# Kernel tuning notes

Measured on AMD Instinct MI355X. Metric: run time of the kernel, lower is better.

## Reference

```python
import jax, jax.numpy as jnp
import numpy as np
from jax import lax

B, S, D = 2, 1024, 1024
N = 16            # mamba state dim
EXPAND = 2
DI = EXPAND * D   # inner dim 2048
K = 4             # depthwise conv kernel
H = 16            # soliton heads
DH = D // H
DT_RANK = D // 16
SOL_DT = 0.1      # soliton integration step


def _ln(x, g, b):
    mu = jnp.mean(x, -1, keepdims=True)
    var = jnp.var(x, -1, keepdims=True)
    return (x - mu) / jnp.sqrt(var + 1e-5) * g + b


def setup_inputs() -> dict:
    key = jax.random.key(0)
    ks = jax.random.split(key, 12)
    def nrm(k, sh, sc=0.02):
        return jax.random.normal(k, sh, jnp.float32) * sc
    return {
        'x': nrm(ks[0], (B, S, D), 1.0),
        'ln1_g': jnp.ones(D), 'ln1_b': jnp.zeros(D),
        'W_in': nrm(ks[1], (D, 2 * DI)), 'b_in': jnp.zeros(2 * DI),
        'conv_w': nrm(ks[2], (DI, K), 0.1), 'conv_b': jnp.zeros(DI),
        'W_xp': nrm(ks[3], (DI, DT_RANK + 2 * N)),
        'W_dt': nrm(ks[4], (DT_RANK, DI), 0.1),
        'b_dt': jnp.full((DI,), -4.6),  # softplus(-4.6) ~ 0.01 init dt
        'A_log': jnp.log(jnp.broadcast_to(jnp.arange(1, N + 1, dtype=jnp.float32), (DI, N))),
        'D_skip': jnp.ones(DI),
        'W_out': nrm(ks[5], (DI, D)), 'b_out': jnp.zeros(D),
        'ln2_g': jnp.ones(D), 'ln2_b': jnp.zeros(D),
        'W_si': nrm(ks[6], (D, D)), 'b_si': jnp.zeros(D),
        'gates': nrm(ks[7], (H, 3), 0.1),   # per-head weights for [sine-Gordon, KdV, Heimburg-Jackson]
        'alpha': nrm(ks[8], (H,), 0.1),     # HJ nonlinearity coefficient
        'W_so': nrm(ks[9], (D, D)), 'b_so': jnp.zeros(D),
    }


def _forward(x, ln1_g, ln1_b, W_in, b_in, conv_w, conv_b, W_xp, W_dt, b_dt,
             A_log, D_skip, W_out, b_out, ln2_g, ln2_b, W_si, b_si,
             gates, alpha, W_so, b_so):
    b, s, d = x.shape
    # ---- Mamba mixer branch ----
    u = _ln(x, ln1_g, ln1_b)
    xz = u @ W_in + b_in                                   # [b,s,2*DI]
    xp, z = jnp.split(xz, 2, axis=-1)                      # [b,s,DI] each
    # causal depthwise conv along sequence
    xt = xp.transpose(0, 2, 1)                             # [b,DI,s]
    yc = lax.conv_general_dilated(xt, conv_w[:, None, :], (1,), [(K - 1, 0)],
                                  feature_group_count=DI,
                                  dimension_numbers=('NCW', 'OIW', 'NCW'))
    xc = jax.nn.silu(yc.transpose(0, 2, 1) + conv_b)       # [b,s,DI]
    dbc = xc @ W_xp
    dtr, Bs, Cs = jnp.split(dbc, [DT_RANK, DT_RANK + N], axis=-1)
    dt = jax.nn.softplus(dtr @ W_dt + b_dt)                # [b,s,DI]
    A = -jnp.exp(A_log)                                    # [DI,N]
    dA = jnp.exp(dt[..., None] * A)                        # [b,s,DI,N]
    dBx = (dt * xc)[..., None] * Bs[:, :, None, :]         # [b,s,DI,N]

    def step(h, inp):
        dA_t, dBx_t, C_t = inp
        h = dA_t * h + dBx_t                               # [b,DI,N]
        y = jnp.einsum('bdn,bn->bd', h, C_t)
        return h, y

    h0 = jnp.zeros((b, DI, N), x.dtype)
    xs = (dA.transpose(1, 0, 2, 3), dBx.transpose(1, 0, 2, 3), Cs.transpose(1, 0, 2))
    _, ys = lax.scan(step, h0, xs)
    y = ys.transpose(1, 0, 2)                              # [b,s,DI]
    y = (y + xc * D_skip) * jax.nn.silu(z)
    x = x + y @ W_out + b_out

    # ---- Soliton interaction branch ----
    v = _ln(x, ln2_g, ln2_b)
    uu = (v @ W_si + b_si).reshape(b, s, H, DH)
    up = jnp.pad(uu, ((0, 0), (2, 2), (0, 0), (0, 0)), mode='edge')
    ux = (up[:, 3:-1] - up[:, 1:-3]) * 0.5                 # central 1st derivative
    uxx = up[:, 3:-1] - 2.0 * uu + up[:, 1:-3]
    uxxx = (up[:, 4:] - 2.0 * up[:, 3:-1] + 2.0 * up[:, 1:-3] - up[:, :-4]) * 0.5
    sg = jnp.sin(uu)                                       # sine-Gordon
    kdv = -6.0 * uu * ux - uxxx                            # KdV
    hj = (1.0 + alpha[None, None, :, None] * uu) * uxx     # Heimburg-Jackson
    du = (gates[None, None, :, 0:1] * sg
          + gates[None, None, :, 1:2] * kdv
          + gates[None, None, :, 2:3] * hj)
    sol = (SOL_DT * du).reshape(b, s, d) @ W_so + b_so
    return x + sol


def reference(x, ln1_g, ln1_b, W_in, b_in, conv_w, conv_b, W_xp, W_dt, b_dt,
              A_log, D_skip, W_out, b_out, ln2_g, ln2_b, W_si, b_si,
              gates, alpha, W_so, b_so):
    return _forward(x, ln1_g, ln1_b, W_in, b_in, conv_w, conv_b, W_xp, W_dt, b_dt,
                    A_log, D_skip, W_out, b_out, ln2_g, ln2_b, W_si, b_si,
                    gates, alpha, W_so, b_so)
```

## Files before the change

### kernel.cpp

```cpp
#include <hip/hip_runtime.h>
#include <hip/hip_bf16.h>
#include <math.h>

typedef unsigned short u16;
typedef unsigned int u32;
typedef __attribute__((ext_vector_type(8))) short short8;
typedef __attribute__((ext_vector_type(4))) float f32x4;

constexpr int CB = 2;
constexpr int CS = 1024;
constexpr int CD = 1024;
constexpr int CDI = 2048;
constexpr int CNC2 = 64;
constexpr int CL2 = 16;

__device__ inline u16 f2bf(float v) {
  __hip_bfloat16 h = __float2bfloat16(v);
  return *reinterpret_cast<u16*>(&h);
}
__device__ inline float bf2f(u16 v) {
  return __uint_as_float(((u32)v) << 16);
}

__device__ inline void gload16(const void* g, void* l) {
  __builtin_amdgcn_global_load_lds((const __attribute__((address_space(1))) void*)g,
                                   (__attribute__((address_space(3))) void*)l, 16, 0, 0);
}

struct TJob { const float* src; u16* dst; int K, N, gx, base; };
struct TJobs { TJob j[6]; };

__global__ __launch_bounds__(256)
void transpose_all_kernel(TJobs jobs) {
  int b = blockIdx.x;
  int ji = 0;
#pragma unroll
  for (int i = 1; i < 6; ++i) if (b >= jobs.j[i].base) ji = i;
  TJob jb = jobs.j[ji];
  int lb = b - jb.base;
  int n0 = (lb % jb.gx) * 32, k0 = (lb / jb.gx) * 32;
  __shared__ float tile[32][33];
  int tx = threadIdx.x & 31, ty = threadIdx.x >> 5;
#pragma unroll
  for (int i = 0; i < 4; ++i) {
    int k = k0 + ty + i * 8, n = n0 + tx;
    tile[ty + i * 8][tx] = (n < jb.N) ? jb.src[(size_t)k * jb.N + n] : 0.f;
  }
  __syncthreads();
#pragma unroll
  for (int i = 0; i < 4; ++i) {
    int n = n0 + ty + i * 8, k = k0 + tx;
    jb.dst[(size_t)n * jb.K + k] = f2bf(tile[tx][ty + i * 8]);
  }
}

__global__ __launch_bounds__(256)
void ln_kernel(const float* __restrict__ x, const float* __restrict__ g,
               const float* __restrict__ bb, u16* __restrict__ outb) {
  int row = blockIdx.x;
  const float4* xr = (const float4*)(x + (size_t)row * CD);
  float4 v = xr[threadIdx.x];
  float s = v.x + v.y + v.z + v.w;
  float ss = v.x * v.x + v.y * v.y + v.z * v.z + v.w * v.w;
#pragma unroll
  for (int o = 1; o < 64; o <<= 1) { s += __shfl_xor(s, o); ss += __shfl_xor(ss, o); }
  __shared__ float sb[4], ssb[4];
  int wid = threadIdx.x >> 6;
  if ((threadIdx.x & 63) == 0) { sb[wid] = s; ssb[wid] = ss; }
  __syncthreads();
  s = sb[0] + sb[1] + sb[2] + sb[3];
  ss = ssb[0] + ssb[1] + ssb[2] + ssb[3];
  float mu = s * (1.f / CD);
  float var = ss * (1.f / CD) - mu * mu;
  float rstd = rsqrtf(var + 1e-5f);
  float4 gv = ((const float4*)g)[threadIdx.x];
  float4 bv = ((const float4*)bb)[threadIdx.x];
  ushort4 o;
  o.x = f2bf((v.x - mu) * rstd * gv.x + bv.x);
  o.y = f2bf((v.y - mu) * rstd * gv.y + bv.y);
  o.z = f2bf((v.z - mu) * rstd * gv.z + bv.z);
  o.w = f2bf((v.w - mu) * rstd * gv.w + bv.w);
  ((ushort4*)(outb + (size_t)row * CD))[threadIdx.x] = o;
}

__global__ __launch_bounds__(256)
void ln_fuse_kernel(const float* __restrict__ x, const u16* __restrict__ S,
                    const float* __restrict__ bo, const float* __restrict__ g,
                    const float* __restrict__ bb, float* __restrict__ out,
                    u16* __restrict__ outb) {
  constexpr size_t SSTR = (size_t)2048 * 1024;
  int row = blockIdx.x;
  float4 xv = ((const float4*)(x + (size_t)row * CD))[threadIdx.x];
  float4 bv0 = ((const float4*)bo)[threadIdx.x];
  float4 v;
  v.x = xv.x + bv0.x; v.y = xv.y + bv0.y; v.z = xv.z + bv0.z; v.w = xv.w + bv0.w;
  size_t base = (size_t)row * CD + threadIdx.x * 4;
#pragma unroll
  for (int z = 0; z < 4; ++z) {
    ushort4 sv = *(const ushort4*)(S + z * SSTR + base);
    v.x += bf2f(sv.x); v.y += bf2f(sv.y); v.z += bf2f(sv.z); v.w += bf2f(sv.w);
  }
  ((float4*)(out + (size_t)row * CD))[threadIdx.x] = v;
  float s = v.x + v.y + v.z + v.w;
  float ss = v.x * v.x + v.y * v.y + v.z * v.z + v.w * v.w;
#pragma unroll
  for (int o = 1; o < 64; o <<= 1) { s += __shfl_xor(s, o); ss += __shfl_xor(ss, o); }
  __shared__ float sb[4], ssb[4];
  int wid = threadIdx.x >> 6;
  if ((threadIdx.x & 63) == 0) { sb[wid] = s; ssb[wid] = ss; }
  __syncthreads();
  s = sb[0] + sb[1] + sb[2] + sb[3];
  ss = ssb[0] + ssb[1] + ssb[2] + ssb[3];
  float mu = s * (1.f / CD);
  float var = ss * (1.f / CD) - mu * mu;
  float rstd = rsqrtf(var + 1e-5f);
  float4 gv = ((const float4*)g)[threadIdx.x];
  float4 bv = ((const float4*)bb)[threadIdx.x];
  ushort4 o;
  o.x = f2bf((v.x - mu) * rstd * gv.x + bv.x);
  o.y = f2bf((v.y - mu) * rstd * gv.y + bv.y);
  o.z = f2bf((v.z - mu) * rstd * gv.z + bv.z);
  o.w = f2bf((v.w - mu) * rstd * gv.w + bv.w);
  ((ushort4*)(outb + (size_t)row * CD))[threadIdx.x] = o;
}

__global__ __launch_bounds__(256)
void add3_kernel(float* __restrict__ out, const u16* __restrict__ S,
                 const float* __restrict__ bias) {
  constexpr size_t SSTR = (size_t)2048 * 1024;
  int idx = blockIdx.x * 256 + threadIdx.x;
  int c4 = idx & 255;
  size_t base = (size_t)idx * 4;
  float4 o = ((const float4*)out)[idx];
  float4 bv = ((const float4*)bias)[c4];
  ushort4 a = *(const ushort4*)(S + base);
  ushort4 b = *(const ushort4*)(S + SSTR + base);
  o.x += bf2f(a.x) + bf2f(b.x) + bv.x;
  o.y += bf2f(a.y) + bf2f(b.y) + bv.y;
  o.z += bf2f(a.z) + bf2f(b.z) + bv.z;
  o.w += bf2f(a.w) + bf2f(b.w) + bv.w;
  ((float4*)out)[idx] = o;
}

template<int BN, int LDA, int LDB>
__global__ __launch_bounds__(256)
void gemm5_kernel(const u16* __restrict__ A, const u16* __restrict__ Bt,
                  const float* __restrict__ bias,
                  const float* __restrict__ resid, int ldr,
                  float* __restrict__ C, int ldc,
                  u16* __restrict__ aux, int auxN,
                  int partial_stride, int Nact, int K, int act) {
  constexpr int WN = BN / 32;
  constexpr int AHALF = 128 * 32;
  constexpr int BHALF = BN * 32;
  __shared__ __align__(16) u16 As[2 * AHALF];
  __shared__ __align__(16) u16 Bs[2 * BHALF];
  const int tid = threadIdx.x, lane = tid & 63, wid = tid >> 6;
  const int wr = wid >> 1, wc = wid & 1;
  int nwg = gridDim.x * gridDim.y;
  int bid = blockIdx.y * gridDim.x + blockIdx.x;
  int swz = (bid & 7) * (nwg >> 3) + (bid >> 3);
  int bx = swz % gridDim.x, by = swz / gridDim.x;
  const int bm = by * 128, bn = bx * BN;
  const int kper = K / gridDim.z;
  const int kbeg = blockIdx.z * kper;
  const int nt = kper / 32;

  int a_src[2], b_src[BN / 64];
#pragma unroll
  for (int j = 0; j < 2; ++j) {
    int c = tid + j * 256;
    int row = c >> 2, kc = (c & 3) ^ ((row + (row >> 2)) & 3);
    a_src[j] = (bm + row) * LDA + kc * 8 + kbeg;
  }
#pragma unroll
  for (int j = 0; j < BN / 64; ++j) {
    int c = tid + j * 256;
    int row = c >> 2, kc = (c & 3) ^ ((row + (row >> 2)) & 3);
    b_src[j] = (bn + row) * LDB + kc * 8 + kbeg;
  }
  int afo[4], bfo[WN];
  const int ch = lane >> 4;
#pragma unroll
  for (int m = 0; m < 4; ++m) {
    int r = wr * 64 + m * 16 + (lane & 15);
    afo[m] = r * 32 + ((ch ^ ((r + (r >> 2)) & 3)) << 3);
  }
#pragma unroll
  for (int n = 0; n < WN; ++n) {
    int r = wc * (BN / 2) + n * 16 + (lane & 15);
    bfo[n] = r * 32 + ((ch ^ ((r + (r >> 2)) & 3)) << 3);
  }
  f32x4 acc[4][WN] = {};

  auto stage = [&](int t, int abuf, int bbuf) {
    int k0 = t * 32;
#pragma unroll
    for (int j = 0; j < 2; ++j)
      gload16(A + a_src[j] + k0, As + abuf + (tid + j * 256) * 8);
#pragma unroll
    for (int j = 0; j < BN / 64; ++j)
      gload16(Bt + b_src[j] + k0, Bs + bbuf + (tid + j * 256) * 8);
  };
  auto compute = [&](int abuf, int bbuf) {
    short8 af[4], bfr[WN];
#pragma unroll
    for (int m = 0; m < 4; ++m) af[m] = *(const short8*)&As[abuf + afo[m]];
#pragma unroll
    for (int n = 0; n < WN; ++n) bfr[n] = *(const short8*)&Bs[bbuf + bfo[n]];
#pragma unroll
    for (int m = 0; m < 4; ++m)
#pragma unroll
      for (int n = 0; n < WN; ++n)
        acc[m][n] = __builtin_amdgcn_mfma_f32_16x16x32_bf16(af[m], bfr[n], acc[m][n], 0, 0, 0);
  };

  stage(0, 0, 0);
  __syncthreads();
  int t = 0;
  while (true) {
    if (t + 1 < nt) stage(t + 1, AHALF, BHALF);
    compute(0, 0);
    __syncthreads();
    if (++t == nt) break;
    if (t + 1 < nt) stage(t + 1, 0, 0);
    compute(AHALF, BHALF);
    __syncthreads();
    if (++t == nt) break;
  }

  const int fr = lane & 15, fq = lane >> 4;
  const int ksegs = gridDim.z;
  u16* Cp = (u16*)C + (size_t)blockIdx.z * partial_stride;
#pragma unroll
  for (int m = 0; m < 4; ++m) {
#pragma unroll
    for (int n = 0; n < WN; ++n) {
#pragma unroll
      for (int j = 0; j < 4; ++j) {
        int row = bm + wr * 64 + m * 16 + fq * 4 + j;
        int col = bn + wc * (BN / 2) + n * 16 + fr;
        if (col < Nact) {
          float v = acc[m][n][j];
          if (ksegs == 1) {
            if (bias) v += bias[col];
            if (resid) v += resid[(size_t)row * ldr + col];
            if (act == 1) v = (v > 20.f) ? v : log1pf(__expf(v));
            if (C) C[(size_t)row * ldc + col] = v;
            if (aux && col < auxN) aux[(size_t)row * auxN + col] = f2bf(v);
          } else if (partial_stride > 0) {
            Cp[(size_t)row * ldc + col] = f2bf(v);
          } else {
            atomicAdd(&C[(size_t)row * ldc + col], v);
          }
        }
      }
    }
  }
}

__global__ __launch_bounds__(256)
void conv_silu_kernel(const u16* __restrict__ xz, const float* __restrict__ w,
                      const float* __restrict__ cb, u16* __restrict__ xcb) {
  int idx = blockIdx.x * 256 + threadIdx.x;
  int d0 = (idx & 255) * 8;
  int t = (idx >> 8) & (CS - 1);
  int b = idx >> 18;
  const u16* base = xz + (size_t)(b * CS) * 4096 + d0;
  float acc[8];
  float4 cb2[2] = { ((const float4*)(cb + d0))[0], ((const float4*)(cb + d0))[1] };
#pragma unroll
  for (int i = 0; i < 8; ++i) acc[i] = ((const float*)cb2)[i];
#pragma unroll
  for (int k = 0; k < 4; ++k) {
    int tt = t - 3 + k;
    if (tt >= 0) {
      short8 v = *(const short8*)(base + (size_t)tt * 4096);
#pragma unroll
      for (int i = 0; i < 8; ++i)
        acc[i] = fmaf(bf2f((u16)v[i]), w[(d0 + i) * 4 + k], acc[i]);
    }
  }
  short8 o;
#pragma unroll
  for (int i = 0; i < 8; ++i) {
    float v = acc[i] * (1.f / (1.f + __expf(-acc[i])));
    o[i] = (short)f2bf(v);
  }
  *(short8*)(xcb + (size_t)(b * CS + t) * CDI + d0) = o;
}

__global__ __launch_bounds__(256)
void dbc_combine_kernel(const u16* __restrict__ parts, float* __restrict__ dbc,
                        u16* __restrict__ dtrb) {
  int idx = blockIdx.x * 256 + threadIdx.x;
  int row = idx / 24, c4 = idx % 24;
  int o = row * 96 + c4 * 4;
  float4 s = make_float4(0.f, 0.f, 0.f, 0.f);
#pragma unroll
  for (int z = 0; z < 16; ++z) {
    ushort4 v = *(const ushort4*)(parts + (size_t)z * (2048 * 96) + o);
    s.x += bf2f(v.x); s.y += bf2f(v.y); s.z += bf2f(v.z); s.w += bf2f(v.w);
  }
  *(float4*)(dbc + o) = s;
  if (c4 < 16) {
    ushort4 b;
    b.x = f2bf(s.x); b.y = f2bf(s.y); b.z = f2bf(s.z); b.w = f2bf(s.w);
    *(ushort4*)(dtrb + row * 64 + c4 * 4) = b;
  }
}

__global__ __launch_bounds__(256)
void scan1_kernel(const u16* __restrict__ dtb, const u16* __restrict__ xcb,
                  const float* __restrict__ dbc, const float* __restrict__ A_log,
                  u16* __restrict__ P, u16* __restrict__ Q) {
  int gid = blockIdx.x * 256 + threadIdx.x;
  int d = gid & (CDI - 1);
  int c = (gid >> 11) & (CNC2 - 1);
  int b = gid >> 17;
  float acoef[16];
#pragma unroll
  for (int j = 0; j < 4; ++j) {
    float4 al = ((const float4*)(A_log + d * 16))[j];
    acoef[j * 4 + 0] = -__expf(al.x);
    acoef[j * 4 + 1] = -__expf(al.y);
    acoef[j * 4 + 2] = -__expf(al.z);
    acoef[j * 4 + 3] = -__expf(al.w);
  }
  float Pv[16], Qv[16];
#pragma unroll
  for (int n = 0; n < 16; ++n) { Pv[n] = 1.f; Qv[n] = 0.f; }
  size_t rowbase = (size_t)b * CS + (size_t)c * CL2;
  for (int i = 0; i < CL2; ++i) {
    size_t r = rowbase + i;
    float dtv = bf2f(dtb[r * CDI + d]);
    float xcv = bf2f(xcb[r * CDI + d]);
    float dx = dtv * xcv;
    const float4* bs4 = (const float4*)(dbc + r * 96 + 64);
    float bs[16];
#pragma unroll
    for (int j = 0; j < 4; ++j) {
      float4 t4 = bs4[j];
      bs[j * 4 + 0] = t4.x; bs[j * 4 + 1] = t4.y; bs[j * 4 + 2] = t4.z; bs[j * 4 + 3] = t4.w;
    }
#pragma unroll
    for (int n = 0; n < 16; ++n) {
      float a = __expf(dtv * acoef[n]);
      Pv[n] *= a;
      Qv[n] = fmaf(a, Qv[n], dx * bs[n]);
    }
  }
  size_t o = (((size_t)b * CNC2 + c) * CDI + d) * 16;
  u16 pb[16], qb[16];
#pragma unroll
  for (int n = 0; n < 16; ++n) { pb[n] = f2bf(Pv[n]); qb[n] = f2bf(Qv[n]); }
#pragma unroll
  for (int j = 0; j < 2; ++j) {
    *(short8*)(P + o + j * 8) = *(short8*)(pb + j * 8);
    *(short8*)(Q + o + j * 8) = *(short8*)(qb + j * 8);
  }
}

__global__ __launch_bounds__(256)
void scan2_kernel(const u16* __restrict__ P, u16* __restrict__ Q) {
  int gid = blockIdx.x * 256 + threadIdx.x;
  int n = gid & 15;
  int d = (gid >> 4) & (CDI - 1);
  int b = gid >> 15;
  int obase = ((b * CNC2) * CDI + d) * 16 + n;
  constexpr int CSTRIDE = CDI * 16;
  float h = 0.f;
  for (int c0 = 0; c0 < CNC2; c0 += 8) {
    float pv[8], qv[8];
#pragma unroll
    for (int i = 0; i < 8; ++i) {
      int o = obase + (c0 + i) * CSTRIDE;
      pv[i] = bf2f(P[o]);
      qv[i] = bf2f(Q[o]);
    }
#pragma unroll
    for (int i = 0; i < 8; ++i) {
      int o = obase + (c0 + i) * CSTRIDE;
      Q[o] = f2bf(h);
      h = fmaf(pv[i], h, qv[i]);
    }
  }
}

__global__ __launch_bounds__(256)
void scan3_kernel(const u16* __restrict__ dtb, const u16* __restrict__ xcb,
                  const float* __restrict__ dbc, const float* __restrict__ A_log,
                  const u16* __restrict__ Q, const u16* __restrict__ xz,
                  const float* __restrict__ Dskip, u16* __restrict__ y2b) {
  int gid = blockIdx.x * 256 + threadIdx.x;
  int d = gid & (CDI - 1);
  int c = (gid >> 11) & (CNC2 - 1);
  int b = gid >> 17;
  float acoef[16];
#pragma unroll
  for (int j = 0; j < 4; ++j) {
    float4 al = ((const float4*)(A_log + d * 16))[j];
    acoef[j * 4 + 0] = -__expf(al.x);
    acoef[j * 4 + 1] = -__expf(al.y);
    acoef[j * 4 + 2] = -__expf(al.z);
    acoef[j * 4 + 3] = -__expf(al.w);
  }
  float h[16];
  size_t o = (((size_t)b * CNC2 + c) * CDI + d) * 16;
#pragma unroll
  for (int j = 0; j < 2; ++j) {
    short8 q8 = *(const short8*)(Q + o + j * 8);
#pragma unroll
    for (int n = 0; n < 8; ++n) h[j * 8 + n] = bf2f((u16)q8[n]);
  }
  float dsk = Dskip[d];
  size_t rowbase = (size_t)b * CS + (size_t)c * CL2;
  for (int i = 0; i < CL2; ++i) {
    size_t r = rowbase + i;
    float dtv = bf2f(dtb[r * CDI + d]);
    float xcv = bf2f(xcb[r * CDI + d]);
    float zv = bf2f(xz[r * 4096 + 2048 + d]);
    float dx = dtv * xcv;
    const float4* bc4 = (const float4*)(dbc + r * 96 + 64);
    float bs[16], cs[16];
#pragma unroll
    for (int j = 0; j < 4; ++j) {
      float4 t4 = bc4[j];
      bs[j * 4 + 0] = t4.x; bs[j * 4 + 1] = t4.y; bs[j * 4 + 2] = t4.z; bs[j * 4 + 3] = t4.w;
      float4 u4 = bc4[4 + j];
      cs[j * 4 + 0] = u4.x; cs[j * 4 + 1] = u4.y; cs[j * 4 + 2] = u4.z; cs[j * 4 + 3] = u4.w;
    }
    float y = 0.f;
#pragma unroll
    for (int n = 0; n < 16; ++n) {
      float a = __expf(dtv * acoef[n]);
      h[n] = fmaf(a, h[n], dx * bs[n]);
      y = fmaf(h[n], cs[n], y);
    }
    float sz = zv * (1.f / (1.f + __expf(-zv)));
    y2b[r * CDI + d] = f2bf((y + xcv * dsk) * sz);
  }
}

__global__ __launch_bounds__(256)
void soliton_kernel(const u16* __restrict__ S, const float* __restrict__ bsi,
                    const float* __restrict__ gates, const float* __restrict__ alpha,
                    u16* __restrict__ sol) {
  constexpr size_t SSTR = (size_t)2048 * 1024;
  int idx = blockIdx.x * 256 + threadIdx.x;
  int d = idx & (CD - 1);
  int t = (idx >> 10) & (CS - 1);
  int b = idx >> 20;
  int h = d >> 6;
  size_t base = (size_t)b * CS * CD + d;
  int tm2 = max(t - 2, 0), tm1 = max(t - 1, 0);
  int tp1 = min(t + 1, CS - 1), tp2 = min(t + 2, CS - 1);
  auto val = [&](int tt) {
    size_t off = base + (size_t)tt * CD;
    return bf2f(S[off]) + bf2f(S[SSTR + off]);
  };
  float um2 = val(tm2);
  float um1 = val(tm1);
  float u0r = val(t);
  float up1 = val(tp1);
  float up2 = val(tp2);
  float u0 = u0r + bsi[d];
  float ux   = (up1 - um1) * 0.5f;
  float uxx  = up1 - 2.f * u0r + um1;
  float uxxx = (up2 - 2.f * up1 + 2.f * um1 - um2) * 0.5f;
  float sg = sinf(u0);
  float kdv = -6.f * u0 * ux - uxxx;
  float hj = (1.f + alpha[h] * u0) * uxx;
  float du = gates[h * 3 + 0] * sg + gates[h * 3 + 1] * kdv + gates[h * 3 + 2] * hj;
  sol[idx] = f2bf(0.1f * du);
}

extern "C" void kernel_launch(void* const* d_in, const int* in_sizes, int n_in,
                              void* d_out, int out_size, void* d_ws, size_t ws_size,
                              hipStream_t stream) {
  const float* x      = (const float*)d_in[0];
  const float* ln1_g  = (const float*)d_in[1];
  const float* ln1_b  = (const float*)d_in[2];
  const float* W_in   = (const float*)d_in[3];
  const float* b_in   = (const float*)d_in[4];
  const float* conv_w = (const float*)d_in[5];
  const float* conv_b = (const float*)d_in[6];
  const float* W_xp   = (const float*)d_in[7];
  const float* W_dt   = (const float*)d_in[8];
  const float* b_dt   = (const float*)d_in[9];
  const float* A_log  = (const float*)d_in[10];
  const float* D_skip = (const float*)d_in[11];
  const float* W_out  = (const float*)d_in[12];
  const float* b_out  = (const float*)d_in[13];
  const float* ln2_g  = (const float*)d_in[14];
  const float* ln2_b  = (const float*)d_in[15];
  const float* W_si   = (const float*)d_in[16];
  const float* b_si   = (const float*)d_in[17];
  const float* gates  = (const float*)d_in[18];
  const float* alpha  = (const float*)d_in[19];
  const float* W_so   = (const float*)d_in[20];
  const float* b_so   = (const float*)d_in[21];
  float* out = (float*)d_out;

  float* ws = (float*)d_ws;
  size_t off = 0;
  auto alloc = [&](size_t nwords) { float* p = ws + off; off += nwords; return p; };
  const size_t BS = (size_t)CB * CS;
  const size_t M1 = 1024 * 1024;

  u16* Wt_in  = (u16*)alloc(2 * M1);
  u16* Wt_xp  = (u16*)alloc(128 * 1024);
  u16* Wt_dt  = (u16*)alloc(64 * 1024);
  u16* Wt_out = (u16*)alloc(M1);
  u16* Wt_si  = (u16*)alloc(M1 / 2);
  u16* Wt_so  = (u16*)alloc(M1 / 2);
  u16* u_bf   = (u16*)alloc(M1);
  u16* sol_bf = u_bf;
  u16* xz_bf  = (u16*)alloc(4 * M1);
  u16* dt_bf  = (u16*)alloc(2 * M1);
  u16* xc_bf  = (u16*)alloc(2 * M1);
  float* dbc  = alloc(BS * 96);
  u16* dtr_bf = (u16*)alloc(64 * 1024);
  float* Pb_f = alloc(2 * M1);
  float* Qb_f = alloc(2 * M1);
  u16* Pb = (u16*)Pb_f;
  u16* Qb = (u16*)Qb_f;
  u16* Slab = (u16*)Pb_f;
  u16* y2_bf  = (u16*)alloc(2 * M1);

  dim3 blk(256);
  const int PSTRIDE = (int)(BS * CD);
  const int DBC_STRIDE = 2048 * 96;

  {
    TJobs jobs;
    int base = 0;
    auto mk = [&](const float* s, u16* dst, int K, int N, int Npad) {
      int gx = Npad / 32, gy = K / 32;
      TJob j{s, dst, K, N, gx, base};
      base += gx * gy;
      return j;
    };
    jobs.j[0] = mk(W_in, Wt_in, 1024, 4096, 4096);
    jobs.j[1] = mk(W_xp, Wt_xp, 2048, 96, 128);
    jobs.j[2] = mk(W_dt, Wt_dt, 64, 2048, 2048);
    jobs.j[3] = mk(W_out, Wt_out, 2048, 1024, 1024);
    jobs.j[4] = mk(W_si, Wt_si, 1024, 1024, 1024);
    jobs.j[5] = mk(W_so, Wt_so, 1024, 1024, 1024);
    transpose_all_kernel<<<base, blk, 0, stream>>>(jobs);
  }

  ln_kernel<<<BS, blk, 0, stream>>>(x, ln1_g, ln1_b, u_bf);
  gemm5_kernel<64, 1024, 1024><<<dim3(64, 16), blk, 0, stream>>>(
      u_bf, Wt_in, b_in, nullptr, 0, nullptr, 0, xz_bf, 4096, 0, 4096, 1024, 0);
  conv_silu_kernel<<<(BS * CDI) / (256 * 8), blk, 0, stream>>>(xz_bf, conv_w, conv_b, xc_bf);
  gemm5_kernel<64, 2048, 2048><<<dim3(2, 16, 16), blk, 0, stream>>>(
      xc_bf, Wt_xp, nullptr, nullptr, 0, (float*)Slab, 96, nullptr, 0, DBC_STRIDE, 96, 2048, 0);
  dbc_combine_kernel<<<(2048 * 24) / 256, blk, 0, stream>>>(Slab, dbc, dtr_bf);
  gemm5_kernel<64, 64, 64><<<dim3(32, 16), blk, 0, stream>>>(
      dtr_bf, Wt_dt, b_dt, nullptr, 0, nullptr, 0, dt_bf, 2048, 0, 2048, 64, 1);
  scan1_kernel<<<(CB * CNC2 * CDI) / 256, blk, 0, stream>>>(dt_bf, xc_bf, dbc, A_log, Pb, Qb);
  scan2_kernel<<<(CB * CDI * 16) / 256, blk, 0, stream>>>(Pb, Qb);
  scan3_kernel<<<(CB * CNC2 * CDI) / 256, blk, 0, stream>>>(dt_bf, xc_bf, dbc, A_log, Qb, xz_bf, D_skip, y2_bf);
  gemm5_kernel<64, 2048, 2048><<<dim3(16, 16, 4), blk, 0, stream>>>(
      y2_bf, Wt_out, nullptr, nullptr, 0, (float*)Slab, CD, nullptr, 0, PSTRIDE, 1024, 2048, 0);
  ln_fuse_kernel<<<BS, blk, 0, stream>>>(x, Slab, b_out, ln2_g, ln2_b, out, u_bf);
  gemm5_kernel<64, 1024, 1024><<<dim3(16, 16, 2), blk, 0, stream>>>(
      u_bf, Wt_si, nullptr, nullptr, 0, (float*)Slab, CD, nullptr, 0, PSTRIDE, 1024, 1024, 0);
  soliton_kernel<<<(BS * CD) / 256, blk, 0, stream>>>(Slab, b_si, gates, alpha, sol_bf);
  gemm5_kernel<64, 1024, 1024><<<dim3(16, 16, 2), blk, 0, stream>>>(
      sol_bf, Wt_so, nullptr, nullptr, 0, (float*)Slab, CD, nullptr, 0, PSTRIDE, 1024, 1024, 0);
  add3_kernel<<<(BS * CD) / (256 * 4), blk, 0, stream>>>(out, Slab, b_so);
}
```

Measured before the change: 247.2 us.

## Triple-buffer GEMM LDS staging with vmcnt-based waits and one barrier

Replaces the double-buffered GEMM main loop with a three-slot LDS ring. Loads run two K-tiles ahead, and each iteration waits on vmcnt(3) followed by a single s_barrier instead of a full __syncthreads after compute. The template is specialised to BN=64, which every call site already used. The goal is to hide more global-load latency and cut one barrier per tile, at the cost of 50% more LDS per block, which may lower occupancy. It also issues redundant clamped loads for the tail tiles.

```diff
diff --git a/kernel.cpp b/kernel.cpp
--- a/kernel.cpp
+++ b/kernel.cpp
@@ -142,44 +142,42 @@
   ((float4*)out)[idx] = o;
 }
 
-template<int BN, int LDA, int LDB>
-__global__ __launch_bounds__(256)
-void gemm5_kernel(const u16* __restrict__ A, const u16* __restrict__ Bt,
+template<int LDA, int LDB>
+__global__ __launch_bounds__(256)
+void gemm7_kernel(const u16* __restrict__ A, const u16* __restrict__ Bt,
                   const float* __restrict__ bias,
                   const float* __restrict__ resid, int ldr,
                   float* __restrict__ C, int ldc,
                   u16* __restrict__ aux, int auxN,
                   int partial_stride, int Nact, int K, int act) {
-  constexpr int WN = BN / 32;
-  constexpr int AHALF = 128 * 32;
-  constexpr int BHALF = BN * 32;
-  __shared__ __align__(16) u16 As[2 * AHALF];
-  __shared__ __align__(16) u16 Bs[2 * BHALF];
+  constexpr int ASLOT = 128 * 32;
+  constexpr int BSLOT = 64 * 32;
+  __shared__ __align__(16) u16 As[3 * ASLOT];
+  __shared__ __align__(16) u16 Bs[3 * BSLOT];
   const int tid = threadIdx.x, lane = tid & 63, wid = tid >> 6;
   const int wr = wid >> 1, wc = wid & 1;
   int nwg = gridDim.x * gridDim.y;
   int bid = blockIdx.y * gridDim.x + blockIdx.x;
   int swz = (bid & 7) * (nwg >> 3) + (bid >> 3);
   int bx = swz % gridDim.x, by = swz / gridDim.x;
-  const int bm = by * 128, bn = bx * BN;
+  const int bm = by * 128, bn = bx * 64;
   const int kper = K / gridDim.z;
   const int kbeg = blockIdx.z * kper;
   const int nt = kper / 32;
 
-  int a_src[2], b_src[BN / 64];
+  int a_src[2], b_src_0;
 #pragma unroll
   for (int j = 0; j < 2; ++j) {
     int c = tid + j * 256;
     int row = c >> 2, kc = (c & 3) ^ ((row + (row >> 2)) & 3);
     a_src[j] = (bm + row) * LDA + kc * 8 + kbeg;
   }
-#pragma unroll
-  for (int j = 0; j < BN / 64; ++j) {
-    int c = tid + j * 256;
+  {
+    int c = tid;
     int row = c >> 2, kc = (c & 3) ^ ((row + (row >> 2)) & 3);
-    b_src[j] = (bn + row) * LDB + kc * 8 + kbeg;
-  }
-  int afo[4], bfo[WN];
+    b_src_0 = (bn + row) * LDB + kc * 8 + kbeg;
+  }
+  int afo[4], bfo[2];
   const int ch = lane >> 4;
 #pragma unroll
   for (int m = 0; m < 4; ++m) {
@@ -187,46 +185,44 @@
     afo[m] = r * 32 + ((ch ^ ((r + (r >> 2)) & 3)) << 3);
   }
 #pragma unroll
-  for (int n = 0; n < WN; ++n) {
-    int r = wc * (BN / 2) + n * 16 + (lane & 15);
+  for (int n = 0; n < 2; ++n) {
+    int r = wc * 32 + n * 16 + (lane & 15);
     bfo[n] = r * 32 + ((ch ^ ((r + (r >> 2)) & 3)) << 3);
   }
-  f32x4 acc[4][WN] = {};
-
-  auto stage = [&](int t, int abuf, int bbuf) {
+  f32x4 acc[4][2] = {};
+
+  auto stage = [&](int t, int slot) {
     int k0 = t * 32;
+    int aoff = slot * ASLOT, boff = slot * BSLOT;
 #pragma unroll
     for (int j = 0; j < 2; ++j)
-      gload16(A + a_src[j] + k0, As + abuf + (tid + j * 256) * 8);
-#pragma unroll
-    for (int j = 0; j < BN / 64; ++j)
-      gload16(Bt + b_src[j] + k0, Bs + bbuf + (tid + j * 256) * 8);
+      gload16(A + a_src[j] + k0, As + aoff + (tid + j * 256) * 8);
+    gload16(Bt + b_src_0 + k0, Bs + boff + tid * 8);
   };
-  auto compute = [&](int abuf, int bbuf) {
-    short8 af[4], bfr[WN];
-#pragma unroll
-    for (int m = 0; m < 4; ++m) af[m] = *(const short8*)&As[abuf + afo[m]];
-#pragma unroll
-    for (int n = 0; n < WN; ++n) bfr[n] = *(const short8*)&Bs[bbuf + bfo[n]];
+  auto compute = [&](int slot) {
+    int aoff = slot * ASLOT, boff = slot * BSLOT;
+    short8 af[4], bfr[2];
+#pragma unroll
+    for (int m = 0; m < 4; ++m) af[m] = *(const short8*)&As[aoff + afo[m]];
+#pragma unroll
+    for (int n = 0; n < 2; ++n) bfr[n] = *(const short8*)&Bs[boff + bfo[n]];
 #pragma unroll
     for (int m = 0; m < 4; ++m)
 #pragma unroll
-      for (int n = 0; n < WN; ++n)
+      for (int n = 0; n < 2; ++n)
         acc[m][n] = __builtin_amdgcn_mfma_f32_16x16x32_bf16(af[m], bfr[n], acc[m][n], 0, 0, 0);
   };
 
-  stage(0, 0, 0);
-  __syncthreads();
-  int t = 0;
-  while (true) {
-    if (t + 1 < nt) stage(t + 1, AHALF, BHALF);
-    compute(0, 0);
-    __syncthreads();
-    if (++t == nt) break;
-    if (t + 1 < nt) stage(t + 1, 0, 0);
-    compute(AHALF, BHALF);
-    __syncthreads();
-    if (++t == nt) break;
+  stage(0, 0);
+  stage(min(1, nt - 1), 1);
+  int s0 = 0, s1 = 1, s2 = 2;
+  for (int t = 0; t < nt; ++t) {
+    asm volatile("s_waitcnt vmcnt(3)" ::: "memory");
+    __builtin_amdgcn_s_barrier();
+    asm volatile("" ::: "memory");
+    stage(min(t + 2, nt - 1), s2);
+    compute(s0);
+    int tmp = s0; s0 = s1; s1 = s2; s2 = tmp;
   }
 
   const int fr = lane & 15, fq = lane >> 4;
@@ -235,11 +231,11 @@
 #pragma unroll
   for (int m = 0; m < 4; ++m) {
 #pragma unroll
-    for (int n = 0; n < WN; ++n) {
+    for (int n = 0; n < 2; ++n) {
 #pragma unroll
       for (int j = 0; j < 4; ++j) {
         int row = bm + wr * 64 + m * 16 + fq * 4 + j;
-        int col = bn + wc * (BN / 2) + n * 16 + fr;
+        int col = bn + wc * 32 + n * 16 + fr;
         if (col < Nact) {
           float v = acc[m][n][j];
           if (ksegs == 1) {
@@ -551,24 +547,24 @@
   }
 
   ln_kernel<<<BS, blk, 0, stream>>>(x, ln1_g, ln1_b, u_bf);
-  gemm5_kernel<64, 1024, 1024><<<dim3(64, 16), blk, 0, stream>>>(
+  gemm7_kernel<1024, 1024><<<dim3(64, 16), blk, 0, stream>>>(
       u_bf, Wt_in, b_in, nullptr, 0, nullptr, 0, xz_bf, 4096, 0, 4096, 1024, 0);
   conv_silu_kernel<<<(BS * CDI) / (256 * 8), blk, 0, stream>>>(xz_bf, conv_w, conv_b, xc_bf);
-  gemm5_kernel<64, 2048, 2048><<<dim3(2, 16, 16), blk, 0, stream>>>(
+  gemm7_kernel<2048, 2048><<<dim3(2, 16, 16), blk, 0, stream>>>(
       xc_bf, Wt_xp, nullptr, nullptr, 0, (float*)Slab, 96, nullptr, 0, DBC_STRIDE, 96, 2048, 0);
   dbc_combine_kernel<<<(2048 * 24) / 256, blk, 0, stream>>>(Slab, dbc, dtr_bf);
-  gemm5_kernel<64, 64, 64><<<dim3(32, 16), blk, 0, stream>>>(
+  gemm7_kernel<64, 64><<<dim3(32, 16), blk, 0, stream>>>(
       dtr_bf, Wt_dt, b_dt, nullptr, 0, nullptr, 0, dt_bf, 2048, 0, 2048, 64, 1);
   scan1_kernel<<<(CB * CNC2 * CDI) / 256, blk, 0, stream>>>(dt_bf, xc_bf, dbc, A_log, Pb, Qb);
   scan2_kernel<<<(CB * CDI * 16) / 256, blk, 0, stream>>>(Pb, Qb);
   scan3_kernel<<<(CB * CNC2 * CDI) / 256, blk, 0, stream>>>(dt_bf, xc_bf, dbc, A_log, Qb, xz_bf, D_skip, y2_bf);
-  gemm5_kernel<64, 2048, 2048><<<dim3(16, 16, 4), blk, 0, stream>>>(
+  gemm7_kernel<2048, 2048><<<dim3(16, 16, 4), blk, 0, stream>>>(
       y2_bf, Wt_out, nullptr, nullptr, 0, (float*)Slab, CD, nullptr, 0, PSTRIDE, 1024, 2048, 0);
   ln_fuse_kernel<<<BS, blk, 0, stream>>>(x, Slab, b_out, ln2_g, ln2_b, out, u_bf);
-  gemm5_kernel<64, 1024, 1024><<<dim3(16, 16, 2), blk, 0, stream>>>(
+  gemm7_kernel<1024, 1024><<<dim3(16, 16, 2), blk, 0, stream>>>(
       u_bf, Wt_si, nullptr, nullptr, 0, (float*)Slab, CD, nullptr, 0, PSTRIDE, 1024, 1024, 0);
   soliton_kernel<<<(BS * CD) / 256, blk, 0, stream>>>(Slab, b_si, gates, alpha, sol_bf);
-  gemm5_kernel<64, 1024, 1024><<<dim3(16, 16, 2), blk, 0, stream>>>(
+  gemm7_kernel<1024, 1024><<<dim3(16, 16, 2), blk, 0, stream>>>(
       sol_bf, Wt_so, nullptr, nullptr, 0, (float*)Slab, CD, nullptr, 0, PSTRIDE, 1024, 1024, 0);
   add3_kernel<<<(BS * CD) / (256 * 4), blk, 0, stream>>>(out, Slab, b_so);
 }
```

Measured after the change: 250.0 us. No clear change (+1.1%).
